# Kernel tuning notes

Measured on AMD Instinct MI355X. Metric: run time of the kernel, lower is better.

## Reference

```python
import jax, jax.numpy as jnp
from jax import lax
import numpy as np

EPS = 1e-5

def _conv(x, w, b, s, p):
    # torch Conv2d: weight [O,I,kH,kW], NCHW
    y = lax.conv_general_dilated(x, w, (s, s), [(p, p), (p, p)],
                                 dimension_numbers=('NCHW', 'OIHW', 'NCHW'))
    return y + b[None, :, None, None]

def _convT(x, w, b, s, p):
    # torch ConvTranspose2d: weight [I,O,kH,kW]; equivalent to lhs-dilated conv
    wf = jnp.flip(w, (2, 3)).transpose(1, 0, 2, 3)  # -> [O,I,kH,kW]
    q = w.shape[2] - 1 - p
    y = lax.conv_general_dilated(x, wf, (1, 1), [(q, q), (q, q)],
                                 lhs_dilation=(s, s),
                                 dimension_numbers=('NCHW', 'OIHW', 'NCHW'))
    return y + b[None, :, None, None]

def _bn(x, g, b, m, v):
    # eval-mode BatchNorm2d with running stats
    s = g / jnp.sqrt(v + EPS)
    return x * s[None, :, None, None] + (b - m * s)[None, :, None, None]

def _forward(x, ew1, eb1, bn1g, bn1b, bn1m, bn1v, ew2, eb2, bn2g, bn2b, bn2m, bn2v,
             ew3, eb3, bn3g, bn3b, bn3m, bn3v, ew4, eb4, bn4g, bn4b, bn4m, bn4v,
             fc21w, fc21b, fc22w, fc22b, fc3w, fc3b,
             cw1, cb1, cbn1g, cbn1b, cbn1m, cbn1v, cw2, cb2, emb,
             dw1, db1, dbn1g, dbn1b, dbn1m, dbn1v, dw2, db2, dbn2g, dbn2b, dbn2m, dbn2v,
             dw3, db3, dbn3g, dbn3b, dbn3m, dbn3v, dw4, db4, dbn4g, dbn4b, dbn4m, dbn4v,
             ow, ob):
    relu = jax.nn.relu
    N = x.shape[0]
    # ---- encoder ----
    h = relu(_bn(_conv(x, ew1, eb1, 2, 1), bn1g, bn1b, bn1m, bn1v))   # [N,16,32,32]
    h = relu(_bn(_conv(h, ew2, eb2, 2, 1), bn2g, bn2b, bn2m, bn2v))   # [N,16,16,16]
    h = relu(_bn(_conv(h, ew3, eb3, 2, 1), bn3g, bn3b, bn3m, bn3v))   # [N,16,9,9]
    h = relu(_bn(_conv(h, ew4, eb4, 1, 0), bn4g, bn4b, bn4m, bn4v))   # [N,128,9,9]
    hl = h.reshape(N, -1)                                              # [N,10368]
    mu = hl @ fc21w + fc21b
    logvar = hl @ fc22w + fc22b
    z = mu  # eval-mode reparameterize returns mu
    # ---- vq_decode ----
    co = relu(z @ fc3w + fc3b)                                         # [N,10368]
    col = co.reshape(N, 128, 9, 9)
    ze = relu(_bn(_convT(col, cw1, cb1, 1, 0), cbn1g, cbn1b, cbn1m, cbn1v))
    z_e_x = _convT(ze, cw2, cb2, 1, 0)                                 # [N,32,9,9]
    zt = z_e_x.transpose(0, 2, 3, 1)                                   # [N,H,W,C]
    # ||z - e||^2 expanded (avoids [N,H,W,C,K] intermediate)
    d = ((zt * zt).sum(-1, keepdims=True)
         - 2.0 * jnp.einsum('nhwc,kc->nhwk', zt, emb)
         + (emb * emb).sum(-1))                                        # [N,H,W,K]
    latents = jnp.argmin(d, axis=-1)                                   # [N,H,W] int
    z_q = emb[latents]                                                 # [N,H,W,C]
    z_q_x = z_q.transpose(0, 3, 1, 2)                                  # [N,32,9,9]
    # ---- decoder ----
    g = relu(_bn(_convT(z_q_x, dw1, db1, 1, 0), dbn1g, dbn1b, dbn1m, dbn1v))  # [N,16,9,9]
    g = relu(_bn(_convT(g, dw2, db2, 2, 1), dbn2g, dbn2b, dbn2m, dbn2v))      # [N,16,18,18]
    g = relu(_bn(_convT(g, dw3, db3, 2, 1), dbn3g, dbn3b, dbn3m, dbn3v))      # [N,16,34,34]
    g = relu(_bn(_convT(g, dw4, db4, 2, 0), dbn4g, dbn4b, dbn4m, dbn4v))      # [N,16,68,68]
    x_tilde = _convT(g, ow, ob, 1, 0)                                         # [N,1,68,68]
    return (x_tilde, z, mu, logvar, z_e_x, z_q_x, latents)


def setup_inputs() -> dict:
    key = jax.random.key(0)
    ks = iter(jax.random.split(key, 64))
    def rn(shape, scale=0.05):
        return scale * jax.random.normal(next(ks), shape, jnp.float32)
    inp = {'x': jax.random.normal(next(ks), (512, 1, 64, 64), jnp.float32)}
    wspecs = {
        'ew1': (16, 1, 4, 4), 'eb1': (16,), 'ew2': (16, 16, 4, 4), 'eb2': (16,),
        'ew3': (16, 16, 2, 2), 'eb3': (16,), 'ew4': (128, 16, 1, 1), 'eb4': (128,),
        'fc21w': (10368, 64), 'fc21b': (64,), 'fc22w': (10368, 64), 'fc22b': (64,),
        'fc3w': (64, 10368), 'fc3b': (10368,),
        'cw1': (128, 32, 1, 1), 'cb1': (32,), 'cw2': (32, 32, 1, 1), 'cb2': (32,),
        'dw1': (32, 16, 1, 1), 'db1': (16,), 'dw2': (16, 16, 4, 4), 'db2': (16,),
        'dw3': (16, 16, 2, 2), 'db3': (16,), 'dw4': (16, 16, 2, 2), 'db4': (16,),
        'ow': (16, 1, 1, 1),
    }
    for n, s in wspecs.items():
        inp[n] = rn(s)
    inp['ob'] = jnp.full((1,), 0.5, jnp.float32)
    for ch, pre in [(16, 'bn1'), (16, 'bn2'), (16, 'bn3'), (128, 'bn4'), (32, 'cbn1'),
                    (16, 'dbn1'), (16, 'dbn2'), (16, 'dbn3'), (16, 'dbn4')]:
        inp[pre + 'g'] = jnp.ones((ch,), jnp.float32)
        inp[pre + 'b'] = jnp.zeros((ch,), jnp.float32)
        inp[pre + 'm'] = jnp.zeros((ch,), jnp.float32)
        inp[pre + 'v'] = jnp.ones((ch,), jnp.float32)
    inp['emb'] = rn((512, 32), 1.0 / 512)
    return inp


def reference(x, ew1, eb1, bn1g, bn1b, bn1m, bn1v, ew2, eb2, bn2g, bn2b, bn2m, bn2v,
              ew3, eb3, bn3g, bn3b, bn3m, bn3v, ew4, eb4, bn4g, bn4b, bn4m, bn4v,
              fc21w, fc21b, fc22w, fc22b, fc3w, fc3b,
              cw1, cb1, cbn1g, cbn1b, cbn1m, cbn1v, cw2, cb2, emb,
              dw1, db1, dbn1g, dbn1b, dbn1m, dbn1v, dw2, db2, dbn2g, dbn2b, dbn2m, dbn2v,
              dw3, db3, dbn3g, dbn3b, dbn3m, dbn3v, dw4, db4, dbn4g, dbn4b, dbn4m, dbn4v,
              ow, ob):
    return _forward(x, ew1, eb1, bn1g, bn1b, bn1m, bn1v, ew2, eb2, bn2g, bn2b, bn2m, bn2v,
                    ew3, eb3, bn3g, bn3b, bn3m, bn3v, ew4, eb4, bn4g, bn4b, bn4m, bn4v,
                    fc21w, fc21b, fc22w, fc22b, fc3w, fc3b,
                    cw1, cb1, cbn1g, cbn1b, cbn1m, cbn1v, cw2, cb2, emb,
                    dw1, db1, dbn1g, dbn1b, dbn1m, dbn1v, dw2, db2, dbn2g, dbn2b, dbn2m, dbn2v,
                    dw3, db3, dbn3g, dbn3b, dbn3m, dbn3v, dw4, db4, dbn4g, dbn4b, dbn4m, dbn4v,
                    ow, ob)
```

## Files before the change

### kernel.cpp

```cpp
#include <hip/hip_runtime.h>
#include <math.h>
#include <float.h>

#define BN_EPS 1e-5f

__device__ __forceinline__ float bn_apply(float y, float g, float b, float m, float v) {
  float s = g / sqrtf(v + BN_EPS);
  return y * s + (b - m * s);
}

__global__ void k_pad0(float* __restrict__ A) {
  int n = blockIdx.x, t = threadIdx.x;
  if (t >= 132) return;
  int r, c;
  if (t < 34)       { r = 0;        c = t; }
  else if (t < 68)  { r = 33;       c = t - 34; }
  else if (t < 100) { r = t - 67;   c = 0; }
  else              { r = t - 99;   c = 33; }
  float4* p = (float4*)(A + n * 18496 + (r * 34 + c) * 16);
  float4 z = make_float4(0.f, 0.f, 0.f, 0.f);
  p[0] = z; p[1] = z; p[2] = z; p[3] = z;
}

__global__ void k_wr2(const float* __restrict__ w, float* __restrict__ wr2) {
  int idx = blockIdx.x * 256 + threadIdx.x;
  int og = idx >> 10, rem = idx & 1023;
  int tap = rem >> 6, r2 = rem & 63;
  int i = r2 >> 2, oo = r2 & 3;
  wr2[idx] = w[(og * 4 + oo) * 256 + i * 16 + tap];
}

__global__ void k_conv1(const float* __restrict__ x, const float* __restrict__ w,
                        const float* __restrict__ bias,
                        const float* __restrict__ g, const float* __restrict__ bb,
                        const float* __restrict__ bm, const float* __restrict__ bv,
                        float* __restrict__ A) {
  int t = blockIdx.x * 256 + threadIdx.x;
  int xo = t & 31, yo = (t >> 5) & 31, n = t >> 10;
  int iy0 = 2 * yo - 1, ix0 = 2 * xo - 1;
  const float* xb = x + n * 4096;
  float p[16];
#pragma unroll
  for (int ky = 0; ky < 4; ++ky)
#pragma unroll
    for (int kx = 0; kx < 4; ++kx) {
      int iy = iy0 + ky, ix = ix0 + kx;
      bool ok = (iy >= 0) & (iy < 64) & (ix >= 0) & (ix < 64);
      p[ky * 4 + kx] = ok ? xb[iy * 64 + ix] : 0.0f;
    }
  float r[16];
#pragma unroll
  for (int o = 0; o < 16; ++o) {
    float acc = bias[o];
#pragma unroll
    for (int k = 0; k < 16; ++k) acc += p[k] * w[o * 16 + k];
    acc = bn_apply(acc, g[o], bb[o], bm[o], bv[o]);
    r[o] = fmaxf(acc, 0.0f);
  }
  float* ob = A + n * 18496 + ((yo + 1) * 34 + (xo + 1)) * 16;
  *(float4*)&ob[0]  = make_float4(r[0], r[1], r[2], r[3]);
  *(float4*)&ob[4]  = make_float4(r[4], r[5], r[6], r[7]);
  *(float4*)&ob[8]  = make_float4(r[8], r[9], r[10], r[11]);
  *(float4*)&ob[12] = make_float4(r[12], r[13], r[14], r[15]);
}

__global__ void __launch_bounds__(256) k_conv2(const float* __restrict__ A,
                        const float* __restrict__ wr2, const float* __restrict__ bias,
                        const float* __restrict__ g, const float* __restrict__ bb,
                        const float* __restrict__ bm, const float* __restrict__ bv,
                        float* __restrict__ out) {
  int t = threadIdx.x;
  int lane = t & 63;
  int og = __builtin_amdgcn_readfirstlane(t >> 6);
  int idx = blockIdx.x * 64 + lane;
  int n = idx >> 8, p = idx & 255;
  int yo = p >> 4, xo = p & 15;
  const float* Ab = A + n * 18496 + (2 * yo * 34 + 2 * xo) * 16;
  const float* wb = wr2 + og * 1024;
  float acc[4];
#pragma unroll
  for (int oo = 0; oo < 4; ++oo) acc[oo] = bias[og * 4 + oo];
#pragma unroll
  for (int ky = 0; ky < 4; ++ky)
#pragma unroll
    for (int kx = 0; kx < 4; ++kx) {
      const float4* tp = (const float4*)(Ab + (ky * 34 + kx) * 16);
      float4 a0 = tp[0], a1 = tp[1], a2 = tp[2], a3 = tp[3];
      const float* wt = wb + (ky * 4 + kx) * 64;
      float pv[16] = {a0.x, a0.y, a0.z, a0.w, a1.x, a1.y, a1.z, a1.w,
                      a2.x, a2.y, a2.z, a2.w, a3.x, a3.y, a3.z, a3.w};
#pragma unroll
      for (int i = 0; i < 16; ++i) {
#pragma unroll
        for (int oo = 0; oo < 4; ++oo)
          acc[oo] = fmaf(pv[i], wt[i * 4 + oo], acc[oo]);
      }
    }
  float* ob = out + n * 4096 + p;
#pragma unroll
  for (int oo = 0; oo < 4; ++oo) {
    int o = og * 4 + oo;
    float s = g[o] / sqrtf(bv[o] + BN_EPS);
    float sh = bb[o] - bm[o] * s;
    ob[o * 256] = fmaxf(acc[oo] * s + sh, 0.0f);
  }
}

__global__ void __launch_bounds__(256) k_c34(const float* __restrict__ in,
    const float* __restrict__ w3, const float* __restrict__ b3,
    const float* __restrict__ g3, const float* __restrict__ bb3,
    const float* __restrict__ bm3, const float* __restrict__ bv3,
    const float* __restrict__ w4, const float* __restrict__ b4,
    const float* __restrict__ g4, const float* __restrict__ bb4,
    const float* __restrict__ bm4, const float* __restrict__ bv4,
    float* __restrict__ hl) {
  __shared__ float xin[4096];
  __shared__ float w3s[1024];
  __shared__ float c3s[16 * 81];
  __shared__ float k3a[16], k3b[16];
  __shared__ float k4a[128], k4b[128];
  int bx = blockIdx.x;
  int n = bx >> 1, half = bx & 1;
  int t = threadIdx.x;
  {
    const float4* iv = (const float4*)(in + n * 4096);
    float4* xv = (float4*)xin;
#pragma unroll
    for (int q = 0; q < 4; ++q) xv[t + 256 * q] = iv[t + 256 * q];
    for (int i = t; i < 1024; i += 256) w3s[i] = w3[i];
  }
  if (t < 16) {
    float s = g3[t] / sqrtf(bv3[t] + BN_EPS);
    k3a[t] = s;
    k3b[t] = b3[t] * s + (bb3[t] - bm3[t] * s);
  } else if (t >= 64 && t < 192) {
    int o = t - 64;
    float s = g4[o] / sqrtf(bv4[o] + BN_EPS);
    k4a[o] = s;
    k4b[o] = b4[o] * s + (bb4[o] - bm4[o] * s);
  }
  __syncthreads();
  for (int idx = t; idx < 1296; idx += 256) {
    int o = idx / 81, p = idx - o * 81;
    int yo = p / 9, xo = p - yo * 9;
    int iy0 = 2 * yo - 1, ix0 = 2 * xo - 1;
    bool ytop = iy0 >= 0, ybot = iy0 + 1 < 16;
    bool xlft = ix0 >= 0, xrgt = ix0 + 1 < 16;
    int iyt = ytop ? iy0 : 0, iyb = ybot ? iy0 + 1 : 15;
    int ixl = xlft ? ix0 : 0, ixr = xrgt ? ix0 + 1 : 15;
    float acc = 0.0f;
#pragma unroll
    for (int i = 0; i < 16; ++i) {
      const float* ch = xin + i * 256;
      float p0 = (ytop & xlft) ? ch[iyt * 16 + ixl] : 0.0f;
      float p1 = (ytop & xrgt) ? ch[iyt * 16 + ixr] : 0.0f;
      float p2 = (ybot & xlft) ? ch[iyb * 16 + ixl] : 0.0f;
      float p3 = (ybot & xrgt) ? ch[iyb * 16 + ixr] : 0.0f;
      float4 wv = *(const float4*)&w3s[(o * 16 + i) * 4];
      acc += p0 * wv.x + p1 * wv.y + p2 * wv.z + p3 * wv.w;
    }
    c3s[idx] = fmaxf(acc * k3a[o] + k3b[o], 0.0f);
  }
  __syncthreads();
  int lane = t & 63;
  int og = __builtin_amdgcn_readfirstlane(t >> 6);
  int o0 = half * 64 + og * 16;
  float* ob = hl + n * 10368;
#pragma unroll
  for (int pass = 0; pass < 2; ++pass) {
    int p = pass * 64 + lane;
    bool ok = p < 81; int pc = ok ? p : 80;
    float acc[16];
#pragma unroll
    for (int oo = 0; oo < 16; ++oo) acc[oo] = 0.0f;
#pragma unroll
    for (int i = 0; i < 16; ++i) {
      float v = c3s[i * 81 + pc];
#pragma unroll
      for (int oo = 0; oo < 16; ++oo)
        acc[oo] = fmaf(v, w4[(o0 + oo) * 16 + i], acc[oo]);
    }
    if (ok) {
#pragma unroll
      for (int oo = 0; oo < 16; ++oo) {
        int o = o0 + oo;
        ob[o * 81 + p] = fmaxf(acc[oo] * k4a[o] + k4b[o], 0.0f);
      }
    }
  }
}

__global__ void __launch_bounds__(256) k_gemm1(const float* __restrict__ hl,
                                               const float* __restrict__ w21,
                                               const float* __restrict__ w22,
                                               float* __restrict__ part) {
  __shared__ __align__(16) float hs[27 * 68];
  __shared__ __align__(16) float wsh[27 * 128];
  int kc = blockIdx.x, nt = blockIdx.y, t = threadIdx.x;
  int n0 = nt * 64, k0 = kc * 162;
  int jg = t & 31, ng = t >> 5;
  float acc[8][4];
#pragma unroll
  for (int i = 0; i < 8; ++i)
#pragma unroll
    for (int q = 0; q < 4; ++q) acc[i][q] = 0.0f;
  float ph[7], pw[14];
  {
    int ks = k0;
#pragma unroll
    for (int q = 0; q < 7; ++q) {
      int idx = t + q * 256;
      if (idx < 1728) { int nr = idx / 27, kk = idx - nr * 27;
        ph[q] = hl[(n0 + nr) * 10368 + ks + kk]; }
    }
#pragma unroll
    for (int q = 0; q < 14; ++q) {
      int idx = t + q * 256;
      if (idx < 3456) { int r = idx >> 7, c = idx & 127;
        pw[q] = (c < 64) ? w21[(ks + r) * 64 + c] : w22[(ks + r) * 64 + (c - 64)]; }
    }
  }
  for (int s = 0; s < 6; ++s) {
    __syncthreads();
#pragma unroll
    for (int q = 0; q < 7; ++q) {
      int idx = t + q * 256;
      if (idx < 1728) { int nr = idx / 27, kk = idx - nr * 27; hs[kk * 68 + nr] = ph[q]; }
    }
#pragma unroll
    for (int q = 0; q < 14; ++q) {
      int idx = t + q * 256;
      if (idx < 3456) wsh[idx] = pw[q];
    }
    __syncthreads();
    if (s < 5) {
      int ks = k0 + (s + 1) * 27;
#pragma unroll
      for (int q = 0; q < 7; ++q) {
        int idx = t + q * 256;
        if (idx < 1728) { int nr = idx / 27, kk = idx - nr * 27;
          ph[q] = hl[(n0 + nr) * 10368 + ks + kk]; }
      }
#pragma unroll
      for (int q = 0; q < 14; ++q) {
        int idx = t + q * 256;
        if (idx < 3456) { int r = idx >> 7, c = idx & 127;
          pw[q] = (c < 64) ? w21[(ks + r) * 64 + c] : w22[(ks + r) * 64 + (c - 64)]; }
      }
    }
#pragma unroll 9
    for (int kk = 0; kk < 27; ++kk) {
      float4 h0 = *(const float4*)&hs[kk * 68 + ng * 8];
      float4 h1 = *(const float4*)&hs[kk * 68 + ng * 8 + 4];
      float4 wv = *(const float4*)&wsh[kk * 128 + jg * 4];
      float hv[8] = {h0.x, h0.y, h0.z, h0.w, h1.x, h1.y, h1.z, h1.w};
#pragma unroll
      for (int i = 0; i < 8; ++i) {
        acc[i][0] = fmaf(hv[i], wv.x, acc[i][0]);
        acc[i][1] = fmaf(hv[i], wv.y, acc[i][1]);
        acc[i][2] = fmaf(hv[i], wv.z, acc[i][2]);
        acc[i][3] = fmaf(hv[i], wv.w, acc[i][3]);
      }
    }
  }
#pragma unroll
  for (int i = 0; i < 8; ++i) {
    int n = n0 + ng * 8 + i;
    *(float4*)&part[(size_t)(kc * 512 + n) * 128 + jg * 4] =
        make_float4(acc[i][0], acc[i][1], acc[i][2], acc[i][3]);
  }
}

__global__ void k_fc_red(const float* __restrict__ part, const float* __restrict__ b21,
                         const float* __restrict__ b22, float* __restrict__ z,
                         float* __restrict__ mu, float* __restrict__ lv) {
  int t = blockIdx.x * 256 + threadIdx.x;
  int j = t & 127, n = t >> 7;
  float s = 0.0f;
  for (int kc = 0; kc < 64; ++kc) s += part[(size_t)(kc * 512 + n) * 128 + j];
  if (j < 64) { float r = s + b21[j]; z[n * 64 + j] = r; mu[n * 64 + j] = r; }
  else        { lv[n * 64 + (j - 64)] = s + b22[j - 64]; }
}

__global__ void k_fc3(const float* __restrict__ z, const float* __restrict__ w,
                      const float* __restrict__ b, float* __restrict__ E) {
  int m = blockIdx.x * 128 + threadIdx.x;
  int n0 = blockIdx.y * 32;
  float acc[32];
#pragma unroll
  for (int nn = 0; nn < 32; ++nn) acc[nn] = 0.0f;
  for (int j = 0; j < 64; ++j) {
    float wv = w[j * 10368 + m];
    const float* zb = z + n0 * 64 + j;
#pragma unroll
    for (int nn = 0; nn < 32; ++nn) acc[nn] += zb[nn * 64] * wv;
  }
  float bvv = b[m];
  float* Eb = E + n0 * 10368 + m;
#pragma unroll
  for (int nn = 0; nn < 32; ++nn) Eb[nn * 10368] = fmaxf(acc[nn] + bvv, 0.0f);
}

__global__ void __launch_bounds__(256) k_cw(const float* __restrict__ E,
                     const float* __restrict__ w1, const float* __restrict__ b1,
                     const float* __restrict__ g, const float* __restrict__ bb,
                     const float* __restrict__ bm, const float* __restrict__ bv,
                     const float* __restrict__ w2, const float* __restrict__ b2,
                     float* __restrict__ zex, float* __restrict__ zt) {
  __shared__ float ze_s[2592];
  int n = blockIdx.x, t = threadIdx.x;
  int lane = t & 63;
  int o0 = __builtin_amdgcn_readfirstlane(t >> 6) * 8;
  const float* co = E + n * 10368;
#pragma unroll
  for (int pass = 0; pass < 2; ++pass) {
    int p = pass * 64 + lane;
    bool ok = p < 81; int pc = ok ? p : 80;
    float acc[8];
#pragma unroll
    for (int oo = 0; oo < 8; ++oo) acc[oo] = b1[o0 + oo];
    for (int i = 0; i < 128; ++i) {
      float v = co[i * 81 + pc];
#pragma unroll
      for (int oo = 0; oo < 8; ++oo)
        acc[oo] = fmaf(v, w1[i * 32 + o0 + oo], acc[oo]);
    }
#pragma unroll
    for (int oo = 0; oo < 8; ++oo) {
      int o = o0 + oo;
      float r = bn_apply(acc[oo], g[o], bb[o], bm[o], bv[o]);
      if (ok) ze_s[o * 81 + p] = fmaxf(r, 0.0f);
    }
  }
  __syncthreads();
  float* zb = zex + n * 2592;
  float* ztb = zt + n * 81 * 32;
#pragma unroll
  for (int pass = 0; pass < 2; ++pass) {
    int p = pass * 64 + lane;
    bool ok = p < 81; int pc = ok ? p : 80;
    float acc[8];
#pragma unroll
    for (int oo = 0; oo < 8; ++oo) acc[oo] = b2[o0 + oo];
    for (int j = 0; j < 32; ++j) {
      float v = ze_s[j * 81 + pc];
#pragma unroll
      for (int oo = 0; oo < 8; ++oo)
        acc[oo] = fmaf(v, w2[j * 32 + o0 + oo], acc[oo]);
    }
    if (ok) {
#pragma unroll
      for (int oo = 0; oo < 8; ++oo) {
        zb[(o0 + oo) * 81 + p] = acc[oo];
        ztb[p * 32 + o0 + oo] = acc[oo];
      }
    }
  }
}

__global__ void k_ee(const float* __restrict__ emb, float* __restrict__ ee) {
  int k = blockIdx.x * 256 + threadIdx.x;
  if (k < 512) {
    const float4* e = (const float4*)(emb + k * 32);
    float s = 0.0f;
#pragma unroll
    for (int q = 0; q < 8; ++q) {
      float4 v = e[q];
      s += v.x * v.x + v.y * v.y + v.z * v.z + v.w * v.w;
    }
    ee[k] = s;
  }
}

__global__ void __launch_bounds__(256) k_vq2(const float* __restrict__ zt,
                                             const float* __restrict__ emb,
                                             const float* __restrict__ ee,
                                             float* __restrict__ lat_out,
                                             float* __restrict__ zqx) {
  __shared__ float bd_s[4][64];
  __shared__ int   bi_s[4][64];
  __shared__ int   bif[64];
  int t = threadIdx.x;
  int lane = t & 63, sub = t >> 6;
  int sub_u = __builtin_amdgcn_readfirstlane(sub);
  int pix = blockIdx.x * 64 + lane;
  float z[32];
  {
    const float4* zr = (const float4*)(zt + (size_t)pix * 32);
#pragma unroll
    for (int q = 0; q < 8; ++q) {
      float4 v = zr[q];
      z[q * 4] = v.x; z[q * 4 + 1] = v.y; z[q * 4 + 2] = v.z; z[q * 4 + 3] = v.w;
    }
  }
  const float* ebase = emb + sub_u * 128 * 32;
  const float* eeb   = ee + sub_u * 128;
  int kbase = sub_u * 128;
  float best = FLT_MAX;
  int bi = kbase;
  for (int kk = 0; kk < 128; kk += 2) {
    const float* e0 = ebase + kk * 32;
    const float* e1 = e0 + 32;
    float d0a = 0.f, d0b = 0.f, d1a = 0.f, d1b = 0.f;
#pragma unroll
    for (int c = 0; c < 32; c += 2) {
      d0a = fmaf(z[c], e0[c], d0a);
      d0b = fmaf(z[c + 1], e0[c + 1], d0b);
      d1a = fmaf(z[c], e1[c], d1a);
      d1b = fmaf(z[c + 1], e1[c + 1], d1b);
    }
    float d0 = fmaf(-2.0f, d0a + d0b, eeb[kk]);
    float d1 = fmaf(-2.0f, d1a + d1b, eeb[kk + 1]);
    if (d0 < best) { best = d0; bi = kbase + kk; }
    if (d1 < best) { best = d1; bi = kbase + kk + 1; }
  }
  bd_s[sub][lane] = best;
  bi_s[sub][lane] = bi;
  __syncthreads();
  if (t < 64) {
    float bd = bd_s[0][t]; int b = bi_s[0][t];
#pragma unroll
    for (int q = 1; q < 4; ++q)
      if (bd_s[q][t] < bd) { bd = bd_s[q][t]; b = bi_s[q][t]; }
    lat_out[blockIdx.x * 64 + t] = (float)b;
    bif[t] = b;
  }
  __syncthreads();
  int pix0 = blockIdx.x * 64;
  for (int idx = t; idx < 2048; idx += 256) {
    int c = idx >> 6, pl = idx & 63;
    int pg = pix0 + pl;
    int n = pg / 81, p = pg - n * 81;
    zqx[n * 2592 + c * 81 + p] = emb[bif[pl] * 32 + c];
  }
}

__global__ void k_dw1(const float* __restrict__ in, const float* __restrict__ w,
                      const float* __restrict__ bias,
                      const float* __restrict__ g, const float* __restrict__ bb,
                      const float* __restrict__ bm, const float* __restrict__ bv,
                      float* __restrict__ out) {
  __shared__ float ws[512];
  for (int i = threadIdx.x; i < 512; i += 256) ws[i] = w[i];
  __syncthreads();
  int t = blockIdx.x * 256 + threadIdx.x;
  int p = t % 81; int o = (t / 81) & 15; int n = t / 1296;
  const float* ib = in + n * 2592 + p;
  float acc = bias[o];
#pragma unroll
  for (int i = 0; i < 32; ++i) acc += ib[i * 81] * ws[i * 16 + o];
  float r = bn_apply(acc, g[o], bb[o], bm[o], bv[o]);
  out[t] = fmaxf(r, 0.0f);
}

__global__ void __launch_bounds__(256) k_dw2(const float* __restrict__ in,
                      const float* __restrict__ w, const float* __restrict__ bias,
                      const float* __restrict__ g, const float* __restrict__ bb,
                      const float* __restrict__ bm, const float* __restrict__ bv,
                      float* __restrict__ out) {
  int t = threadIdx.x;
  int lane = t & 63;
  int og = __builtin_amdgcn_readfirstlane(t >> 6);
  int idx = blockIdx.x * 64 + lane;
  int n = idx / 81, blk = idx - n * 81;
  int iy = blk / 9, ix = blk - iy * 9;
  const float* ib = in + n * 1296;
  int r0 = iy - 1, r2 = iy + 1, c0 = ix - 1, c2 = ix + 1;
  bool r0ok = r0 >= 0, r2ok = r2 < 9, c0ok = c0 >= 0, c2ok = c2 < 9;
  int r0c = r0ok ? r0 : 0, r2c = r2ok ? r2 : 8;
  int c0c = c0ok ? c0 : 0, c2c = c2ok ? c2 : 8;
  float acc[4][2][2];
#pragma unroll
  for (int oo = 0; oo < 4; ++oo)
#pragma unroll
    for (int dy = 0; dy < 2; ++dy)
#pragma unroll
      for (int dx = 0; dx < 2; ++dx) acc[oo][dy][dx] = 0.0f;
  for (int i = 0; i < 16; ++i) {
    const float* ch = ib + i * 81;
    float v[3][3];
    v[1][1] = ch[iy * 9 + ix];
    v[1][0] = c0ok ? ch[iy * 9 + c0c] : 0.0f;
    v[1][2] = c2ok ? ch[iy * 9 + c2c] : 0.0f;
    v[0][1] = r0ok ? ch[r0c * 9 + ix] : 0.0f;
    v[0][0] = (r0ok & c0ok) ? ch[r0c * 9 + c0c] : 0.0f;
    v[0][2] = (r0ok & c2ok) ? ch[r0c * 9 + c2c] : 0.0f;
    v[2][1] = r2ok ? ch[r2c * 9 + ix] : 0.0f;
    v[2][0] = (r2ok & c0ok) ? ch[r2c * 9 + c0c] : 0.0f;
    v[2][2] = (r2ok & c2ok) ? ch[r2c * 9 + c2c] : 0.0f;
    const float* wb = w + (i * 16 + og * 4) * 16;
#pragma unroll
    for (int oo = 0; oo < 4; ++oo) {
      const float* wo = wb + oo * 16;
      acc[oo][0][0] = fmaf(v[1][1], wo[1 * 4 + 1], acc[oo][0][0]);
      acc[oo][0][0] = fmaf(v[1][0], wo[1 * 4 + 3], acc[oo][0][0]);
      acc[oo][0][0] = fmaf(v[0][1], wo[3 * 4 + 1], acc[oo][0][0]);
      acc[oo][0][0] = fmaf(v[0][0], wo[3 * 4 + 3], acc[oo][0][0]);
      acc[oo][0][1] = fmaf(v[1][1], wo[1 * 4 + 2], acc[oo][0][1]);
      acc[oo][0][1] = fmaf(v[1][2], wo[1 * 4 + 0], acc[oo][0][1]);
      acc[oo][0][1] = fmaf(v[0][1], wo[3 * 4 + 2], acc[oo][0][1]);
      acc[oo][0][1] = fmaf(v[0][2], wo[3 * 4 + 0], acc[oo][0][1]);
      acc[oo][1][0] = fmaf(v[1][1], wo[2 * 4 + 1], acc[oo][1][0]);
      acc[oo][1][0] = fmaf(v[1][0], wo[2 * 4 + 3], acc[oo][1][0]);
      acc[oo][1][0] = fmaf(v[2][1], wo[0 * 4 + 1], acc[oo][1][0]);
      acc[oo][1][0] = fmaf(v[2][0], wo[0 * 4 + 3], acc[oo][1][0]);
      acc[oo][1][1] = fmaf(v[1][1], wo[2 * 4 + 2], acc[oo][1][1]);
      acc[oo][1][1] = fmaf(v[1][2], wo[2 * 4 + 0], acc[oo][1][1]);
      acc[oo][1][1] = fmaf(v[2][1], wo[0 * 4 + 2], acc[oo][1][1]);
      acc[oo][1][1] = fmaf(v[2][2], wo[0 * 4 + 0], acc[oo][1][1]);
    }
  }
  float* ob = out + n * 5184 + (2 * iy) * 18 + 2 * ix;
#pragma unroll
  for (int oo = 0; oo < 4; ++oo) {
    int o = og * 4 + oo;
    float s = g[o] / sqrtf(bv[o] + BN_EPS);
    float sh = bb[o] - bm[o] * s;
    float bo = bias[o];
    float r00 = fmaxf((acc[oo][0][0] + bo) * s + sh, 0.0f);
    float r01 = fmaxf((acc[oo][0][1] + bo) * s + sh, 0.0f);
    float r10 = fmaxf((acc[oo][1][0] + bo) * s + sh, 0.0f);
    float r11 = fmaxf((acc[oo][1][1] + bo) * s + sh, 0.0f);
    float* op = ob + o * 324;
    *(float2*)&op[0]  = make_float2(r00, r01);
    *(float2*)&op[18] = make_float2(r10, r11);
  }
}

__global__ void k_dw3(const float* __restrict__ in, const float* __restrict__ w,
                      const float* __restrict__ bias,
                      const float* __restrict__ g, const float* __restrict__ bb,
                      const float* __restrict__ bm, const float* __restrict__ bv,
                      float* __restrict__ out) {
  int t = blockIdx.x * 256 + threadIdx.x;
  int ii = t % 324; int n = t / 324;
  int iy = ii / 18, ix = ii % 18;
  const float* ib = in + n * 5184 + iy * 18 + ix;
  float acc[4][16];
#pragma unroll
  for (int a = 0; a < 4; ++a)
#pragma unroll
    for (int o = 0; o < 16; ++o) acc[a][o] = 0.0f;
  for (int i = 0; i < 16; ++i) {
    float v = ib[i * 324];
    const float4* wr = (const float4*)(w + i * 64);
#pragma unroll
    for (int o = 0; o < 16; ++o) {
      float4 wt = wr[o];
      acc[0][o] = fmaf(v, wt.x, acc[0][o]);
      acc[1][o] = fmaf(v, wt.y, acc[1][o]);
      acc[2][o] = fmaf(v, wt.z, acc[2][o]);
      acc[3][o] = fmaf(v, wt.w, acc[3][o]);
    }
  }
  int yo0 = 2 * iy - 1, xo0 = 2 * ix - 1;
  float* ob = out + n * 18496;
#pragma unroll
  for (int o = 0; o < 16; ++o) {
    float s = g[o] / sqrtf(bv[o] + BN_EPS);
    float sh = bb[o] - bm[o] * s;
    float bo = bias[o];
#pragma unroll
    for (int a = 0; a < 2; ++a)
#pragma unroll
      for (int b = 0; b < 2; ++b) {
        int yo = yo0 + a, xo = xo0 + b;
        if (yo >= 0 && yo < 34 && xo >= 0 && xo < 34)
          ob[o * 1156 + yo * 34 + xo] = fmaxf((acc[a * 2 + b][o] + bo) * s + sh, 0.0f);
      }
  }
}

__global__ void k_dw4ow(const float* __restrict__ in, const float* __restrict__ w,
                        const float* __restrict__ bias,
                        const float* __restrict__ g, const float* __restrict__ bb,
                        const float* __restrict__ bm, const float* __restrict__ bv,
                        const float* __restrict__ oww, const float* __restrict__ obb,
                        float* __restrict__ out) {
  int t = blockIdx.x * 256 + threadIdx.x;
  int ii = t % 1156; int n = t / 1156;
  int iy = ii / 34, ix = ii % 34;
  const float* ib = in + n * 18496 + iy * 34 + ix;
  float acc[4][16];
#pragma unroll
  for (int a = 0; a < 4; ++a)
#pragma unroll
    for (int o = 0; o < 16; ++o) acc[a][o] = 0.0f;
  for (int i = 0; i < 16; ++i) {
    float v = ib[i * 1156];
    const float4* wr = (const float4*)(w + i * 64);
#pragma unroll
    for (int o = 0; o < 16; ++o) {
      float4 wt = wr[o];
      acc[0][o] = fmaf(v, wt.x, acc[0][o]);
      acc[1][o] = fmaf(v, wt.y, acc[1][o]);
      acc[2][o] = fmaf(v, wt.z, acc[2][o]);
      acc[3][o] = fmaf(v, wt.w, acc[3][o]);
    }
  }
  float r[4];
#pragma unroll
  for (int a = 0; a < 4; ++a) r[a] = obb[0];
#pragma unroll
  for (int o = 0; o < 16; ++o) {
    float s = g[o] / sqrtf(bv[o] + BN_EPS);
    float sh = bb[o] - bm[o] * s;
    float bo = bias[o];
    float wo = oww[o];
#pragma unroll
    for (int a = 0; a < 4; ++a)
      r[a] += fmaxf((acc[a][o] + bo) * s + sh, 0.0f) * wo;
  }
  float* ob = out + n * 4624 + 2 * ix;
  *(float2*)&ob[(2 * iy) * 68]     = make_float2(r[0], r[1]);
  *(float2*)&ob[(2 * iy + 1) * 68] = make_float2(r[2], r[3]);
}

extern "C" void kernel_launch(void* const* d_in, const int* in_sizes, int n_in,
                              void* d_out, int out_size, void* d_ws, size_t ws_size,
                              hipStream_t stream) {
  const float* x     = (const float*)d_in[0];
  const float* ew1   = (const float*)d_in[1];
  const float* eb1   = (const float*)d_in[2];
  const float* ew2   = (const float*)d_in[3];
  const float* eb2   = (const float*)d_in[4];
  const float* ew3   = (const float*)d_in[5];
  const float* eb3   = (const float*)d_in[6];
  const float* ew4   = (const float*)d_in[7];
  const float* eb4   = (const float*)d_in[8];
  const float* fc21w = (const float*)d_in[9];
  const float* fc21b = (const float*)d_in[10];
  const float* fc22w = (const float*)d_in[11];
  const float* fc22b = (const float*)d_in[12];
  const float* fc3w  = (const float*)d_in[13];
  const float* fc3b  = (const float*)d_in[14];
  const float* cw1   = (const float*)d_in[15];
  const float* cb1   = (const float*)d_in[16];
  const float* cw2   = (const float*)d_in[17];
  const float* cb2   = (const float*)d_in[18];
  const float* dw1   = (const float*)d_in[19];
  const float* db1   = (const float*)d_in[20];
  const float* dw2   = (const float*)d_in[21];
  const float* db2   = (const float*)d_in[22];
  const float* dw3   = (const float*)d_in[23];
  const float* db3   = (const float*)d_in[24];
  const float* dw4   = (const float*)d_in[25];
  const float* db4   = (const float*)d_in[26];
  const float* oww   = (const float*)d_in[27];
  const float* obb   = (const float*)d_in[28];
  const float* bn1g  = (const float*)d_in[29];
  const float* bn1b  = (const float*)d_in[30];
  const float* bn1m  = (const float*)d_in[31];
  const float* bn1v  = (const float*)d_in[32];
  const float* bn2g  = (const float*)d_in[33];
  const float* bn2b  = (const float*)d_in[34];
  const float* bn2m  = (const float*)d_in[35];
  const float* bn2v  = (const float*)d_in[36];
  const float* bn3g  = (const float*)d_in[37];
  const float* bn3b  = (const float*)d_in[38];
  const float* bn3m  = (const float*)d_in[39];
  const float* bn3v  = (const float*)d_in[40];
  const float* bn4g  = (const float*)d_in[41];
  const float* bn4b  = (const float*)d_in[42];
  const float* bn4m  = (const float*)d_in[43];
  const float* bn4v  = (const float*)d_in[44];
  const float* cbn1g = (const float*)d_in[45];
  const float* cbn1b = (const float*)d_in[46];
  const float* cbn1m = (const float*)d_in[47];
  const float* cbn1v = (const float*)d_in[48];
  const float* dbn1g = (const float*)d_in[49];
  const float* dbn1b = (const float*)d_in[50];
  const float* dbn1m = (const float*)d_in[51];
  const float* dbn1v = (const float*)d_in[52];
  const float* dbn2g = (const float*)d_in[53];
  const float* dbn2b = (const float*)d_in[54];
  const float* dbn2m = (const float*)d_in[55];
  const float* dbn2v = (const float*)d_in[56];
  const float* dbn3g = (const float*)d_in[57];
  const float* dbn3b = (const float*)d_in[58];
  const float* dbn3m = (const float*)d_in[59];
  const float* dbn3v = (const float*)d_in[60];
  const float* dbn4g = (const float*)d_in[61];
  const float* dbn4b = (const float*)d_in[62];
  const float* dbn4m = (const float*)d_in[63];
  const float* dbn4v = (const float*)d_in[64];
  const float* emb   = (const float*)d_in[65];

  float* out = (float*)d_out;
  float* xt_o  = out;
  float* z_o   = out + 2367488;
  float* mu_o  = out + 2400256;
  float* lv_o  = out + 2433024;
  float* zex_o = out + 2465792;
  float* zqx_o = out + 3792896;
  float* lat_o = out + 5120000;

  float* ws = (float*)d_ws;
  float* A    = ws;
  float* Bt   = ws + 9469952;
  float* Dhl  = ws;
  float* part = ws + 9469952;
  float* Eco  = ws;
  float* zt   = ws + 9469952;
  float* G    = ws + 9469952;
  float* H    = ws + 10133504;
  float* I    = ws;
  float* eev  = ws + 13664256;
  float* wr2  = ws + 13664768;

  k_pad0<<<512, 256, 0, stream>>>(A);
  k_wr2<<<16, 256, 0, stream>>>(ew2, wr2);
  k_conv1<<<2048, 256, 0, stream>>>(x, ew1, eb1, bn1g, bn1b, bn1m, bn1v, A);
  k_conv2<<<2048, 256, 0, stream>>>(A, wr2, eb2, bn2g, bn2b, bn2m, bn2v, Bt);
  k_c34<<<1024, 256, 0, stream>>>(Bt, ew3, eb3, bn3g, bn3b, bn3m, bn3v,
                                  ew4, eb4, bn4g, bn4b, bn4m, bn4v, Dhl);
  k_gemm1<<<dim3(64, 8), 256, 0, stream>>>(Dhl, fc21w, fc22w, part);
  k_fc_red<<<256, 256, 0, stream>>>(part, fc21b, fc22b, z_o, mu_o, lv_o);
  k_ee<<<2, 256, 0, stream>>>(emb, eev);
  k_fc3<<<dim3(81, 16), 128, 0, stream>>>(z_o, fc3w, fc3b, Eco);
  k_cw<<<512, 256, 0, stream>>>(Eco, cw1, cb1, cbn1g, cbn1b, cbn1m, cbn1v, cw2, cb2, zex_o, zt);
  k_vq2<<<648, 256, 0, stream>>>(zt, emb, eev, lat_o, zqx_o);
  k_dw1<<<2592, 256, 0, stream>>>(zqx_o, dw1, db1, dbn1g, dbn1b, dbn1m, dbn1v, G);
  k_dw2<<<648, 256, 0, stream>>>(G, dw2, db2, dbn2g, dbn2b, dbn2m, dbn2v, H);
  k_dw3<<<648, 256, 0, stream>>>(H, dw3, db3, dbn3g, dbn3b, dbn3m, dbn3v, I);
  k_dw4ow<<<2312, 256, 0, stream>>>(I, dw4, db4, dbn4g, dbn4b, dbn4m, dbn4v, oww, obb, xt_o);
}
```

Measured before the change: 501.8 us.

## Switch conv1 output to channel-planar padded layout and compute all 16 channels per thread

The padded conv1 activation buffer changes from channel-interleaved (NHWC-like, 16 floats per pixel) to channel-planar (per-channel 34x34 planes). conv2 now has each thread compute all 16 output channels, reading float2 pairs from each input channel plane and the original weight layout directly. This removes the weight-reorder kernel and cuts the conv2 grid by four. In exchange it loses the float4 vector loads, and conv1's stores become scalar and strided across planes.

```diff
diff --git a/kernel.cpp b/kernel.cpp
--- a/kernel.cpp
+++ b/kernel.cpp
@@ -11,23 +11,16 @@
 
 __global__ void k_pad0(float* __restrict__ A) {
   int n = blockIdx.x, t = threadIdx.x;
-  if (t >= 132) return;
-  int r, c;
-  if (t < 34)       { r = 0;        c = t; }
-  else if (t < 68)  { r = 33;       c = t - 34; }
-  else if (t < 100) { r = t - 67;   c = 0; }
-  else              { r = t - 99;   c = 33; }
-  float4* p = (float4*)(A + n * 18496 + (r * 34 + c) * 16);
-  float4 z = make_float4(0.f, 0.f, 0.f, 0.f);
-  p[0] = z; p[1] = z; p[2] = z; p[3] = z;
-}
-
-__global__ void k_wr2(const float* __restrict__ w, float* __restrict__ wr2) {
-  int idx = blockIdx.x * 256 + threadIdx.x;
-  int og = idx >> 10, rem = idx & 1023;
-  int tap = rem >> 6, r2 = rem & 63;
-  int i = r2 >> 2, oo = r2 & 3;
-  wr2[idx] = w[(og * 4 + oo) * 256 + i * 16 + tap];
+  float* ab = A + n * 18496;
+  for (int idx = t; idx < 2112; idx += 256) {
+    int ch = idx / 132, b = idx - ch * 132;
+    int r, c;
+    if (b < 34)       { r = 0;      c = b; }
+    else if (b < 68)  { r = 33;     c = b - 34; }
+    else if (b < 100) { r = b - 67; c = 0; }
+    else              { r = b - 99; c = 33; }
+    ab[ch * 1156 + r * 34 + c] = 0.0f;
+  }
 }
 
 __global__ void k_conv1(const float* __restrict__ x, const float* __restrict__ w,
@@ -48,61 +41,53 @@
       bool ok = (iy >= 0) & (iy < 64) & (ix >= 0) & (ix < 64);
       p[ky * 4 + kx] = ok ? xb[iy * 64 + ix] : 0.0f;
     }
-  float r[16];
+  float* ob = A + n * 18496 + (yo + 1) * 34 + (xo + 1);
 #pragma unroll
   for (int o = 0; o < 16; ++o) {
     float acc = bias[o];
 #pragma unroll
     for (int k = 0; k < 16; ++k) acc += p[k] * w[o * 16 + k];
     acc = bn_apply(acc, g[o], bb[o], bm[o], bv[o]);
-    r[o] = fmaxf(acc, 0.0f);
-  }
-  float* ob = A + n * 18496 + ((yo + 1) * 34 + (xo + 1)) * 16;
-  *(float4*)&ob[0]  = make_float4(r[0], r[1], r[2], r[3]);
-  *(float4*)&ob[4]  = make_float4(r[4], r[5], r[6], r[7]);
-  *(float4*)&ob[8]  = make_float4(r[8], r[9], r[10], r[11]);
-  *(float4*)&ob[12] = make_float4(r[12], r[13], r[14], r[15]);
+    ob[o * 1156] = fmaxf(acc, 0.0f);
+  }
 }
 
 __global__ void __launch_bounds__(256) k_conv2(const float* __restrict__ A,
-                        const float* __restrict__ wr2, const float* __restrict__ bias,
+                        const float* __restrict__ w, const float* __restrict__ bias,
                         const float* __restrict__ g, const float* __restrict__ bb,
                         const float* __restrict__ bm, const float* __restrict__ bv,
                         float* __restrict__ out) {
-  int t = threadIdx.x;
-  int lane = t & 63;
-  int og = __builtin_amdgcn_readfirstlane(t >> 6);
-  int idx = blockIdx.x * 64 + lane;
+  int idx = blockIdx.x * 256 + threadIdx.x;
   int n = idx >> 8, p = idx & 255;
   int yo = p >> 4, xo = p & 15;
-  const float* Ab = A + n * 18496 + (2 * yo * 34 + 2 * xo) * 16;
-  const float* wb = wr2 + og * 1024;
-  float acc[4];
-#pragma unroll
-  for (int oo = 0; oo < 4; ++oo) acc[oo] = bias[og * 4 + oo];
-#pragma unroll
-  for (int ky = 0; ky < 4; ++ky)
-#pragma unroll
-    for (int kx = 0; kx < 4; ++kx) {
-      const float4* tp = (const float4*)(Ab + (ky * 34 + kx) * 16);
-      float4 a0 = tp[0], a1 = tp[1], a2 = tp[2], a3 = tp[3];
-      const float* wt = wb + (ky * 4 + kx) * 64;
-      float pv[16] = {a0.x, a0.y, a0.z, a0.w, a1.x, a1.y, a1.z, a1.w,
-                      a2.x, a2.y, a2.z, a2.w, a3.x, a3.y, a3.z, a3.w};
-#pragma unroll
-      for (int i = 0; i < 16; ++i) {
-#pragma unroll
-        for (int oo = 0; oo < 4; ++oo)
-          acc[oo] = fmaf(pv[i], wt[i * 4 + oo], acc[oo]);
-      }
-    }
+  const float* Ab = A + n * 18496 + (2 * yo) * 34 + 2 * xo;
+  float acc[16];
+#pragma unroll
+  for (int o = 0; o < 16; ++o) acc[o] = bias[o];
+  for (int i = 0; i < 16; ++i) {
+    const float* ch = Ab + i * 1156;
+    float pv[16];
+#pragma unroll
+    for (int ky = 0; ky < 4; ++ky) {
+      float2 a = *(const float2*)(ch + ky * 34);
+      float2 b = *(const float2*)(ch + ky * 34 + 2);
+      pv[ky * 4 + 0] = a.x; pv[ky * 4 + 1] = a.y;
+      pv[ky * 4 + 2] = b.x; pv[ky * 4 + 3] = b.y;
+    }
+    const float* wi = w + i * 16;
+#pragma unroll
+    for (int o = 0; o < 16; ++o) {
+      const float* wo = wi + o * 256;
+#pragma unroll
+      for (int k = 0; k < 16; ++k) acc[o] = fmaf(pv[k], wo[k], acc[o]);
+    }
+  }
   float* ob = out + n * 4096 + p;
 #pragma unroll
-  for (int oo = 0; oo < 4; ++oo) {
-    int o = og * 4 + oo;
+  for (int o = 0; o < 16; ++o) {
     float s = g[o] / sqrtf(bv[o] + BN_EPS);
     float sh = bb[o] - bm[o] * s;
-    ob[o * 256] = fmaxf(acc[oo] * s + sh, 0.0f);
+    ob[o * 256] = fmaxf(acc[o] * s + sh, 0.0f);
   }
 }
 
@@ -706,12 +691,10 @@
   float* H    = ws + 10133504;
   float* I    = ws;
   float* eev  = ws + 13664256;
-  float* wr2  = ws + 13664768;
 
   k_pad0<<<512, 256, 0, stream>>>(A);
-  k_wr2<<<16, 256, 0, stream>>>(ew2, wr2);
   k_conv1<<<2048, 256, 0, stream>>>(x, ew1, eb1, bn1g, bn1b, bn1m, bn1v, A);
-  k_conv2<<<2048, 256, 0, stream>>>(A, wr2, eb2, bn2g, bn2b, bn2m, bn2v, Bt);
+  k_conv2<<<512, 256, 0, stream>>>(A, ew2, eb2, bn2g, bn2b, bn2m, bn2v, Bt);
   k_c34<<<1024, 256, 0, stream>>>(Bt, ew3, eb3, bn3g, bn3b, bn3m, bn3v,
                                   ew4, eb4, bn4g, bn4b, bn4m, bn4v, Dhl);
   k_gemm1<<<dim3(64, 8), 256, 0, stream>>>(Dhl, fc21w, fc22w, part);
```

New measurement: 503.2 us. About the same (+0.3%).
